# Kernel optimization log

Hardware: AMD Instinct MI355X
Metric: run time of the kernel (lower is better)

The kernel has to match this reference:

```python
import jax, jax.numpy as jnp
import numpy as np

H, W, B, D, N = 256, 256, 200, 128, 1024
NEG_SLOPE = 0.01  # nn.LeakyReLU default

def lrelu(x):
    return jnp.where(x > 0, x, NEG_SLOPE * x)

def setup_inputs() -> dict:
    key = jax.random.key(0)
    ks = jax.random.split(key, 12)
    x = jax.random.normal(ks[0], (H, W, B), dtype=jnp.float32)
    # pixel->superpixel soft assignment (nonnegative)
    Q = jax.random.uniform(ks[1], (H * W, N), dtype=jnp.float32)
    # sparse-ish symmetric superpixel adjacency
    a = (jax.random.uniform(ks[2], (N, N)) < 0.05).astype(jnp.float32)
    adj = jnp.maximum(a, a.T)
    s = 0.05
    params = {
        'bn0_g': jnp.ones((B,), jnp.float32), 'bn0_b': jnp.zeros((B,), jnp.float32),
        'w1': s * jax.random.normal(ks[3], (B, D), jnp.float32), 'b1': jnp.zeros((D,), jnp.float32),
        'bn1_g': jnp.ones((D,), jnp.float32), 'bn1_b': jnp.zeros((D,), jnp.float32),
        'w2': s * jax.random.normal(ks[4], (D, D), jnp.float32), 'b2': jnp.zeros((D,), jnp.float32),
        'gcn_bn_g': jnp.ones((3, D), jnp.float32), 'gcn_bn_b': jnp.zeros((3, D), jnp.float32),
        'gcn_w': s * jax.random.normal(ks[5], (3, D, D), jnp.float32),
        'gcn_b': jnp.zeros((3, D), jnp.float32),
    }
    return dict(x=x, Q=Q, adj=adj, **params)

def reference(x, Q, adj, bn0_g, bn0_b, w1, b1, bn1_g, bn1_b, w2, b2,
              gcn_bn_g, gcn_bn_b, gcn_w, gcn_b):
    h_, w_, _ = x.shape
    # CNN_denoise: BN2d + 1x1 conv (== per-pixel matmul) x2, LeakyReLU
    t = bn0_g * x + bn0_b                      # eval-mode BN (identity running stats)
    t = lrelu(jnp.einsum('hwb,bd->hwd', t, w1) + b1)
    t = bn1_g * t + bn1_b
    t = lrelu(jnp.einsum('hwd,de->hwe', t, w2) + b2)
    xf = t.reshape(h_ * w_, -1)                # [HW, D]
    # superpixel pooling with column-normalized Q
    normQ = Q / jnp.sum(Q, axis=0, keepdims=True)
    h = normQ.T @ xf                           # [N, D]
    # symmetric-normalized adjacency (A + I), computed once (same for all layers)
    g = adj + jnp.eye(adj.shape[0], dtype=adj.dtype)
    dinv = jnp.sum(g, axis=1) ** -0.5
    gn = dinv[:, None] * g * dinv[None, :]     # D^-1/2 (A+I) D^-1/2
    for i in range(3):                         # 3 GCN layers (structural loop)
        hb = gcn_bn_g[i] * h + gcn_bn_b[i]     # BatchNorm1d, eval mode
        h = lrelu((gn @ hb) @ gcn_w[i] + gcn_b[i])
    # write superpixel features back to pixels
    out = Q @ h                                # [HW, D]
    return out
```

## Files before the change

kernel.cpp:

```cpp
#include <hip/hip_runtime.h>

#define HWP 65536
#define NSP 1024
#define DCH 128
#define KC  64
#define JC  16

typedef float f32x4 __attribute__((ext_vector_type(4)));
typedef short bf16x8 __attribute__((ext_vector_type(8)));
typedef short bf16x4 __attribute__((ext_vector_type(4)));

__device__ __forceinline__ float lrelu(float v) { return v > 0.f ? v : 0.01f * v; }

__device__ __forceinline__ short f2bf(float f) {
    __bf16 h = (__bf16)f;
    return __builtin_bit_cast(short, h);
}

__device__ __forceinline__ void cvtA(bf16x8 (&bf)[4], const float (&src)[4][8])
{
#pragma unroll
    for (int mf = 0; mf < 4; ++mf)
#pragma unroll
        for (int j = 0; j < 8; ++j) bf[mf][j] = f2bf(src[mf][j]);
}

__global__ __launch_bounds__(256) void prep_w(
    const float* __restrict__ w1, const float* __restrict__ b1,
    const float* __restrict__ bn0_g, const float* __restrict__ bn0_b,
    const float* __restrict__ w2, const float* __restrict__ b2,
    const float* __restrict__ bn1_g, const float* __restrict__ bn1_b,
    short* __restrict__ w1t, short* __restrict__ w2t,
    float* __restrict__ b1f, float* __restrict__ b2f)
{
    int t = blockIdx.x * 256 + threadIdx.x;
    if (t < 7 * 8 * 64 * 8) {
        int j = t & 7, lane = (t >> 3) & 63, nf = (t >> 9) & 7, ks = t >> 12;
        int ch = ks * 32 + (lane >> 4) * 8 + j;
        int d  = nf * 16 + (lane & 15);
        float v = (ch < 200) ? bn0_g[ch] * w1[ch * 128 + d] : 0.f;
        w1t[t] = f2bf(v);
    }
    if (t < 4 * 8 * 64 * 8) {
        int j = t & 7, lane = (t >> 3) & 63, nf = (t >> 9) & 7, ks = t >> 12;
        int k = ks * 32 + (lane >> 4) * 8 + j;
        int d = nf * 16 + (lane & 15);
        w2t[t] = f2bf(bn1_g[k] * w2[k * 128 + d]);
    }
    if (t < 128) {
        float s1 = b1[t], s2 = b2[t];
        for (int ch = 0; ch < 200; ++ch) s1 += bn0_b[ch] * w1[ch * 128 + t];
        for (int k = 0; k < 128; ++k)   s2 += bn1_b[k] * w2[k * 128 + t];
        b1f[t] = s1; b2f[t] = s2;
    }
}

__global__ __launch_bounds__(128) void cnn_mfma(
    const float* __restrict__ x, const short* __restrict__ w1t,
    const float* __restrict__ b1f, const short* __restrict__ w2t,
    const float* __restrict__ b2f, short* __restrict__ xfT)
{
    __shared__ __align__(16) short a2[2][4][4][64][8];
    const int t = threadIdx.x;
    const int w = t >> 6, l = t & 63;
    const int q = l >> 4, li = l & 15;
    const int pix0 = blockIdx.x * 128 + w * 64;

    f32x4 acc[4][8];
#pragma unroll
    for (int nf = 0; nf < 8; ++nf) {
        float bv = b1f[nf * 16 + li];
#pragma unroll
        for (int mf = 0; mf < 4; ++mf) acc[mf][nf] = (f32x4){bv, bv, bv, bv};
    }

    for (int ks = 0; ks < 7; ++ks) {
        bf16x8 a[4];
        if (ks < 6 || q == 0) {
            int k0 = ks * 32 + q * 8;
#pragma unroll
            for (int mf = 0; mf < 4; ++mf) {
                const float* sp = &x[(size_t)(pix0 + mf * 16 + li) * 200 + k0];
                float4 u = *(const float4*)sp;
                float4 v = *(const float4*)(sp + 4);
                a[mf][0] = f2bf(u.x); a[mf][1] = f2bf(u.y);
                a[mf][2] = f2bf(u.z); a[mf][3] = f2bf(u.w);
                a[mf][4] = f2bf(v.x); a[mf][5] = f2bf(v.y);
                a[mf][6] = f2bf(v.z); a[mf][7] = f2bf(v.w);
            }
        } else {
#pragma unroll
            for (int mf = 0; mf < 4; ++mf)
#pragma unroll
                for (int j = 0; j < 8; ++j) a[mf][j] = 0;
        }
#pragma unroll
        for (int nf = 0; nf < 8; ++nf) {
            bf16x8 b = *(const bf16x8*)&w1t[((ks * 8 + nf) * 64 + l) * 8];
#pragma unroll
            for (int mf = 0; mf < 4; ++mf)
                acc[mf][nf] = __builtin_amdgcn_mfma_f32_16x16x32_bf16(a[mf], b, acc[mf][nf], 0, 0, 0);
        }
    }

#pragma unroll
    for (int mf = 0; mf < 4; ++mf)
#pragma unroll
        for (int nf = 0; nf < 8; ++nf)
#pragma unroll
            for (int j = 0; j < 4; ++j) {
                float v = lrelu(acc[mf][nf][j]);
                int row = mf * 16 + q * 4 + j;
                int col = nf * 16 + li;
                int ks2 = col >> 5;
                int lane2 = (row & 15) + (((col & 31) >> 3) << 4);
                a2[w][ks2][mf][lane2][col & 7] = f2bf(v);
            }
    __syncthreads();

    f32x4 acc2[4][8];
#pragma unroll
    for (int nf = 0; nf < 8; ++nf) {
        float bv = b2f[nf * 16 + li];
#pragma unroll
        for (int mf = 0; mf < 4; ++mf) acc2[mf][nf] = (f32x4){bv, bv, bv, bv};
    }
#pragma unroll
    for (int ks = 0; ks < 4; ++ks) {
        bf16x8 a[4];
#pragma unroll
        for (int mf = 0; mf < 4; ++mf)
            a[mf] = *(const bf16x8*)&a2[w][ks][mf][l][0];
#pragma unroll
        for (int nf = 0; nf < 8; ++nf) {
            bf16x8 b = *(const bf16x8*)&w2t[((ks * 8 + nf) * 64 + l) * 8];
#pragma unroll
            for (int mf = 0; mf < 4; ++mf)
                acc2[mf][nf] = __builtin_amdgcn_mfma_f32_16x16x32_bf16(a[mf], b, acc2[mf][nf], 0, 0, 0);
        }
    }

#pragma unroll
    for (int mf = 0; mf < 4; ++mf)
#pragma unroll
        for (int nf = 0; nf < 8; ++nf) {
            bf16x4 p;
#pragma unroll
            for (int j = 0; j < 4; ++j) p[j] = f2bf(lrelu(acc2[mf][nf][j]));
            int d2 = nf * 16 + li;
            int pix = pix0 + mf * 16 + q * 4;
            *(bf16x4*)&xfT[(size_t)d2 * HWP + pix] = p;
        }
}

__device__ __forceinline__ void pool_loadA(float (&dst)[4][8], const float* __restrict__ Q,
                                           int rbase, int ncol0)
{
#pragma unroll
    for (int mf = 0; mf < 4; ++mf) {
        const float* sp = &Q[(size_t)rbase * NSP + ncol0 + mf * 16];
#pragma unroll
        for (int j = 0; j < 8; ++j) dst[mf][j] = sp[(size_t)j * NSP];
    }
}
__device__ __forceinline__ void pool_loadB(bf16x8 (&dst)[4], const short* __restrict__ xfT,
                                           int dcol0, int rbase)
{
#pragma unroll
    for (int nf = 0; nf < 4; ++nf)
        dst[nf] = *(const bf16x8*)&xfT[(size_t)(dcol0 + nf * 16) * HWP + rbase];
}

__global__ __launch_bounds__(256, 2) void pool_mfma(
    const float* __restrict__ Q, const short* __restrict__ xfT,
    float* __restrict__ P_part, float* __restrict__ qs_part)
{
    const int t = threadIdx.x;
    const int wid = t >> 6, l = t & 63;
    const int q = l >> 4, li = l & 15;
    const int n0 = blockIdx.x * 128 + (wid >> 1) * 64;
    const int d0 = (wid & 1) * 64;
    const int chunk = blockIdx.y;
    const int r0 = chunk * 1024;
    const int ncol0 = n0 + li;
    const int dcol0 = d0 + li;

    f32x4 acc[4][4];
    f32x4 accq[4];
#pragma unroll
    for (int mf = 0; mf < 4; ++mf) {
        accq[mf] = (f32x4){0.f, 0.f, 0.f, 0.f};
#pragma unroll
        for (int nf = 0; nf < 4; ++nf) acc[mf][nf] = (f32x4){0.f, 0.f, 0.f, 0.f};
    }
    bf16x8 bone;
    {
        short onev = (li == 0) ? (short)0x3F80 : (short)0;
#pragma unroll
        for (int j = 0; j < 8; ++j) bone[j] = onev;
    }

    float a0[4][8], a1[4][8];
    bf16x8 b0[4], b1v[4];
    pool_loadA(a0, Q, r0 + q * 8, ncol0);
    pool_loadB(b0, xfT, dcol0, r0 + q * 8);

    for (int ks = 0; ks < 32; ks += 2) {
        pool_loadA(a1, Q, r0 + (ks + 1) * 32 + q * 8, ncol0);
        pool_loadB(b1v, xfT, dcol0, r0 + (ks + 1) * 32 + q * 8);
        {
            bf16x8 abf[4]; cvtA(abf, a0);
#pragma unroll
            for (int mf = 0; mf < 4; ++mf) {
#pragma unroll
                for (int nf = 0; nf < 4; ++nf)
                    acc[mf][nf] = __builtin_amdgcn_mfma_f32_16x16x32_bf16(abf[mf], b0[nf], acc[mf][nf], 0, 0, 0);
                if (d0 == 0)
                    accq[mf] = __builtin_amdgcn_mfma_f32_16x16x32_bf16(abf[mf], bone, accq[mf], 0, 0, 0);
            }
        }
        if (ks + 2 < 32) {
            pool_loadA(a0, Q, r0 + (ks + 2) * 32 + q * 8, ncol0);
            pool_loadB(b0, xfT, dcol0, r0 + (ks + 2) * 32 + q * 8);
        }
        {
            bf16x8 abf[4]; cvtA(abf, a1);
#pragma unroll
            for (int mf = 0; mf < 4; ++mf) {
#pragma unroll
                for (int nf = 0; nf < 4; ++nf)
                    acc[mf][nf] = __builtin_amdgcn_mfma_f32_16x16x32_bf16(abf[mf], b1v[nf], acc[mf][nf], 0, 0, 0);
                if (d0 == 0)
                    accq[mf] = __builtin_amdgcn_mfma_f32_16x16x32_bf16(abf[mf], bone, accq[mf], 0, 0, 0);
            }
        }
    }

#pragma unroll
    for (int mf = 0; mf < 4; ++mf)
#pragma unroll
        for (int nf = 0; nf < 4; ++nf)
#pragma unroll
            for (int j = 0; j < 4; ++j) {
                int n = n0 + mf * 16 + q * 4 + j;
                int d = d0 + nf * 16 + li;
                P_part[((size_t)chunk * NSP + n) * DCH + d] = acc[mf][nf][j];
            }
    if (d0 == 0 && li == 0)
#pragma unroll
        for (int mf = 0; mf < 4; ++mf)
#pragma unroll
            for (int j = 0; j < 4; ++j)
                qs_part[chunk * NSP + n0 + mf * 16 + q * 4 + j] = accq[mf][j];
}

__global__ __launch_bounds__(256) void reduce_h0(
    const float* __restrict__ P_part, const float* __restrict__ qs_part,
    float* __restrict__ h)
{
    const int i4 = blockIdx.x * 256 + threadIdx.x;
    const int n = i4 >> 5;
    f32x4 s = (f32x4){0.f, 0.f, 0.f, 0.f};
    const f32x4* P4 = (const f32x4*)P_part;
    for (int k = 0; k < KC; ++k) s += P4[(size_t)k * (NSP * DCH / 4) + i4];
    float qs = 0.f;
    for (int k = 0; k < KC; ++k) qs += qs_part[k * NSP + n];
    float inv = 1.f / qs;
    ((f32x4*)h)[i4] = s * inv;
}

__global__ __launch_bounds__(256) void dinv_k(const float* __restrict__ adj,
                                              float* __restrict__ dinv)
{
    __shared__ float red[256];
    const int n = blockIdx.x;
    const int t = threadIdx.x;
    float4 v = *(const float4*)&adj[(size_t)n * NSP + t * 4];
    red[t] = v.x + v.y + v.z + v.w;
    __syncthreads();
    for (int off = 128; off > 0; off >>= 1) {
        if (t < off) red[t] += red[t + off];
        __syncthreads();
    }
    if (t == 0) dinv[n] = rsqrtf(red[0] + 1.0f);
}

__global__ __launch_bounds__(256) void m1_k(
    const float* __restrict__ adj, const float* __restrict__ h,
    const float* __restrict__ dinv, const float* __restrict__ gg,
    const float* __restrict__ gb, float* __restrict__ m1p)
{
    __shared__ float adjL[16][64];
    __shared__ float hbL[64][128];
    const int r0 = blockIdx.x * 16;
    const int jc = blockIdx.y;
    const int j0 = jc * 64;
    const int t = threadIdx.x;
    const int d = t & 127, ph = t >> 7;

    for (int i = t; i < 16 * 64; i += 256) {
        int row = i >> 6, col = i & 63;
        adjL[row][col] = adj[(size_t)(r0 + row) * NSP + j0 + col];
    }
    for (int i = t; i < 64 * 128; i += 256) {
        int jr = i >> 7, dd = i & 127;
        int j = j0 + jr;
        hbL[jr][dd] = dinv[j] * (gg[dd] * h[(size_t)j * DCH + dd] + gb[dd]);
    }
    __syncthreads();

    float acc[8];
#pragma unroll
    for (int pp = 0; pp < 8; ++pp) acc[pp] = 0.f;
    for (int jj = 0; jj < 64; ++jj) {
        float hv = hbL[jj][d];
#pragma unroll
        for (int pp = 0; pp < 8; ++pp)
            acc[pp] += adjL[ph * 8 + pp][jj] * hv;
    }
#pragma unroll
    for (int pp = 0; pp < 8; ++pp)
        m1p[(size_t)jc * (NSP * DCH) + (size_t)(r0 + ph * 8 + pp) * DCH + d] = acc[pp];
}

__global__ __launch_bounds__(256) void gcnw_k(
    const float* __restrict__ m1p, const float* __restrict__ h,
    const float* __restrict__ dinv, const float* __restrict__ gg,
    const float* __restrict__ gb, const float* __restrict__ W,
    const float* __restrict__ bias, float* __restrict__ hout)
{
    __shared__ float ms[16 * 128];
    __shared__ float WL[64 * 128];
    const int r0 = blockIdx.x * 16;
    const int t = threadIdx.x;
    for (int i = t; i < 2048; i += 256) {
        int r = r0 + (i >> 7), dd = i & 127;
        float hbr = dinv[r] * (gg[dd] * h[(size_t)r * DCH + dd] + gb[dd]);
        float s = hbr;
#pragma unroll
        for (int kc = 0; kc < JC; ++kc)
            s += m1p[(size_t)kc * (NSP * DCH) + (size_t)r0 * DCH + i];
        ms[i] = dinv[r] * s;
    }
    const int e = t & 127, ph = t >> 7;
    float acc[8];
#pragma unroll
    for (int pp = 0; pp < 8; ++pp) acc[pp] = bias[e];
    for (int sub = 0; sub < 2; ++sub) {
        __syncthreads();
        for (int i = t; i < 64 * 128; i += 256)
            WL[i] = W[(size_t)sub * 64 * 128 + i];
        __syncthreads();
        for (int dd = 0; dd < 64; ++dd) {
            float wv = WL[dd * 128 + e];
#pragma unroll
            for (int pp = 0; pp < 8; ++pp)
                acc[pp] += ms[(ph * 8 + pp) * 128 + sub * 64 + dd] * wv;
        }
    }
#pragma unroll
    for (int pp = 0; pp < 8; ++pp)
        hout[(size_t)(r0 + ph * 8 + pp) * DCH + e] = lrelu(acc[pp]);
}

__global__ __launch_bounds__(256) void htprep(const float* __restrict__ h,
                                              short* __restrict__ htb)
{
    int t = blockIdx.x * 256 + threadIdx.x;
    int j = t & 7, lane = (t >> 3) & 63, nf = (t >> 9) & 7, ks = t >> 12;
    htb[t] = f2bf(h[(ks * 32 + (lane >> 4) * 8 + j) * 128 + nf * 16 + (lane & 15)]);
}

__device__ __forceinline__ void out_loadA(float (&dst)[4][8], const float* __restrict__ Q,
                                          int rrow0, int k0)
{
#pragma unroll
    for (int mf = 0; mf < 4; ++mf) {
        const float* sp = &Q[(size_t)(rrow0 + mf * 16) * NSP + k0];
        float4 u = *(const float4*)sp;
        float4 v = *(const float4*)(sp + 4);
        dst[mf][0] = u.x; dst[mf][1] = u.y; dst[mf][2] = u.z; dst[mf][3] = u.w;
        dst[mf][4] = v.x; dst[mf][5] = v.y; dst[mf][6] = v.z; dst[mf][7] = v.w;
    }
}
__device__ __forceinline__ void out_loadB(bf16x8 (&dst)[4], const short* __restrict__ htb,
                                          int ks, int nfbase, int l)
{
#pragma unroll
    for (int nf = 0; nf < 4; ++nf)
        dst[nf] = *(const bf16x8*)&htb[((ks * 8 + nfbase + nf) * 64 + l) * 8];
}

__global__ __launch_bounds__(256, 2) void out_mfma(
    const float* __restrict__ Q, const short* __restrict__ htb,
    float* __restrict__ out)
{
    const int t = threadIdx.x;
    const int wid = t >> 6, l = t & 63;
    const int q = l >> 4, li = l & 15;
    const int r0 = blockIdx.x * 128 + (wid >> 1) * 64;
    const int d0 = (wid & 1) * 64;
    const int rrow0 = r0 + li;
    const int nfb = d0 >> 4;

    f32x4 acc[4][4];
#pragma unroll
    for (int mf = 0; mf < 4; ++mf)
#pragma unroll
        for (int nf = 0; nf < 4; ++nf) acc[mf][nf] = (f32x4){0.f, 0.f, 0.f, 0.f};

    float a0[4][8], a1[4][8];
    bf16x8 b0[4], b1v[4];
    out_loadA(a0, Q, rrow0, q * 8);
    out_loadB(b0, htb, 0, nfb, l);

    for (int ks = 0; ks < 32; ks += 2) {
        out_loadA(a1, Q, rrow0, (ks + 1) * 32 + q * 8);
        out_loadB(b1v, htb, ks + 1, nfb, l);
        {
            bf16x8 abf[4]; cvtA(abf, a0);
#pragma unroll
            for (int mf = 0; mf < 4; ++mf)
#pragma unroll
                for (int nf = 0; nf < 4; ++nf)
                    acc[mf][nf] = __builtin_amdgcn_mfma_f32_16x16x32_bf16(abf[mf], b0[nf], acc[mf][nf], 0, 0, 0);
        }
        if (ks + 2 < 32) {
            out_loadA(a0, Q, rrow0, (ks + 2) * 32 + q * 8);
            out_loadB(b0, htb, ks + 2, nfb, l);
        }
        {
            bf16x8 abf[4]; cvtA(abf, a1);
#pragma unroll
            for (int mf = 0; mf < 4; ++mf)
#pragma unroll
                for (int nf = 0; nf < 4; ++nf)
                    acc[mf][nf] = __builtin_amdgcn_mfma_f32_16x16x32_bf16(abf[mf], b1v[nf], acc[mf][nf], 0, 0, 0);
        }
    }

#pragma unroll
    for (int mf = 0; mf < 4; ++mf)
#pragma unroll
        for (int nf = 0; nf < 4; ++nf)
#pragma unroll
            for (int j = 0; j < 4; ++j)
                out[(size_t)(r0 + mf * 16 + q * 4 + j) * DCH + d0 + nf * 16 + li] = acc[mf][nf][j];
}

extern "C" void kernel_launch(void* const* d_in, const int* in_sizes, int n_in,
                              void* d_out, int out_size, void* d_ws, size_t ws_size,
                              hipStream_t stream)
{
    const float* x      = (const float*)d_in[0];
    const float* Q      = (const float*)d_in[1];
    const float* adj    = (const float*)d_in[2];
    const float* bn0_g  = (const float*)d_in[3];
    const float* bn0_b  = (const float*)d_in[4];
    const float* w1     = (const float*)d_in[5];
    const float* b1     = (const float*)d_in[6];
    const float* bn1_g  = (const float*)d_in[7];
    const float* bn1_b  = (const float*)d_in[8];
    const float* w2     = (const float*)d_in[9];
    const float* b2     = (const float*)d_in[10];
    const float* gbn_g  = (const float*)d_in[11];
    const float* gbn_b  = (const float*)d_in[12];
    const float* gcn_w  = (const float*)d_in[13];
    const float* gcn_b  = (const float*)d_in[14];

    float* out = (float*)d_out;
    float* ws  = (float*)d_ws;

    float* P_part  = ws;
    float* qs_part = P_part + (size_t)KC * NSP * DCH;
    float* hA      = qs_part + (size_t)KC * NSP;
    float* hB      = hA + NSP * DCH;
    float* dinvb   = hB + NSP * DCH;
    short* htb     = (short*)(dinvb + NSP);
    short* w1t     = (short*)((float*)htb + 65536);
    short* w2t     = (short*)((float*)w1t + 14336);
    float* b1f     = (float*)w2t + 8192;
    float* b2f     = b1f + 128;
    float* m1p     = P_part;
    short* xfT     = (short*)d_out;

    prep_w<<<112, 256, 0, stream>>>(w1, b1, bn0_g, bn0_b, w2, b2, bn1_g, bn1_b,
                                    w1t, w2t, b1f, b2f);
    cnn_mfma<<<HWP / 128, 128, 0, stream>>>(x, w1t, b1f, w2t, b2f, xfT);
    pool_mfma<<<dim3(NSP / 128, KC), 256, 0, stream>>>(Q, xfT, P_part, qs_part);
    reduce_h0<<<(NSP * DCH / 4) / 256, 256, 0, stream>>>(P_part, qs_part, hA);
    dinv_k<<<NSP, 256, 0, stream>>>(adj, dinvb);

    const float* hcur = hA;
    float* hnext = hB;
    for (int i = 0; i < 3; ++i) {
        m1_k<<<dim3(NSP / 16, JC), 256, 0, stream>>>(adj, hcur, dinvb,
                                                     gbn_g + i * DCH, gbn_b + i * DCH, m1p);
        gcnw_k<<<NSP / 16, 256, 0, stream>>>(m1p, hcur, dinvb,
                                             gbn_g + i * DCH, gbn_b + i * DCH,
                                             gcn_w + (size_t)i * DCH * DCH,
                                             gcn_b + i * DCH, hnext);
        const float* tmp = hcur;
        hcur = hnext;
        hnext = (float*)tmp;
    }

    htprep<<<(NSP * DCH) / 256, 256, 0, stream>>>(hcur, htb);
    out_mfma<<<HWP / 128, 256, 0, stream>>>(Q, htb, out);
}
```

Before: 316.6 us.

## Stage Q tiles into LDS via async global_load_lds with double buffering

The out_mfma kernel previously had each wave load its own Q rows straight into registers, so the two waves sharing a row range fetched the same Q data twice. It now stages each 128x64 Q tile into a double-buffered, XOR-swizzled shared-memory buffer with global_load_lds, and waves read their fragments from LDS. This is meant to halve global Q traffic and overlap the next tile's load with MFMA work. In exchange it uses 64KB of LDS per block, which may limit occupancy, and adds a barrier per tile.

```diff
diff --git a/kernel.cpp b/kernel.cpp
--- a/kernel.cpp
+++ b/kernel.cpp
@@ -371,36 +371,42 @@
     htb[t] = f2bf(h[(ks * 32 + (lane >> 4) * 8 + j) * 128 + nf * 16 + (lane & 15)]);
 }
 
-__device__ __forceinline__ void out_loadA(float (&dst)[4][8], const float* __restrict__ Q,
-                                          int rrow0, int k0)
-{
-#pragma unroll
-    for (int mf = 0; mf < 4; ++mf) {
-        const float* sp = &Q[(size_t)(rrow0 + mf * 16) * NSP + k0];
-        float4 u = *(const float4*)sp;
-        float4 v = *(const float4*)(sp + 4);
-        dst[mf][0] = u.x; dst[mf][1] = u.y; dst[mf][2] = u.z; dst[mf][3] = u.w;
-        dst[mf][4] = v.x; dst[mf][5] = v.y; dst[mf][6] = v.z; dst[mf][7] = v.w;
-    }
-}
 __device__ __forceinline__ void out_loadB(bf16x8 (&dst)[4], const short* __restrict__ htb,
                                           int ks, int nfbase, int l)
 {
 #pragma unroll
     for (int nf = 0; nf < 4; ++nf)
         dst[nf] = *(const bf16x8*)&htb[((ks * 8 + nfbase + nf) * 64 + l) * 8];
+}
+
+__device__ __forceinline__ void stage_q(const float* __restrict__ Q, float* dst,
+                                        int r0, int kbase, int wid, int l)
+{
+#pragma unroll
+    for (int i = 0; i < 8; ++i) {
+        int o = (i * 4 + wid) * 1024 + l * 16;
+        int row = o >> 8;
+        int bin = o & 255;
+        const float* src = Q + (size_t)(r0 + row) * NSP + kbase
+                             + ((bin ^ ((row & 7) << 5)) >> 2);
+        __builtin_amdgcn_global_load_lds(
+            (const __attribute__((address_space(1))) unsigned int*)src,
+            (__attribute__((address_space(3))) unsigned int*)(dst + (o >> 2)),
+            16, 0, 0);
+    }
 }
 
 __global__ __launch_bounds__(256, 2) void out_mfma(
     const float* __restrict__ Q, const short* __restrict__ htb,
     float* __restrict__ out)
 {
+    __shared__ __align__(16) float qs[2][8192];
     const int t = threadIdx.x;
     const int wid = t >> 6, l = t & 63;
     const int q = l >> 4, li = l & 15;
-    const int r0 = blockIdx.x * 128 + (wid >> 1) * 64;
+    const int r0 = blockIdx.x * 128;
+    const int rw = (wid >> 1) * 64;
     const int d0 = (wid & 1) * 64;
-    const int rrow0 = r0 + li;
     const int nfb = d0 >> 4;
 
     f32x4 acc[4][4];
@@ -409,33 +415,53 @@
 #pragma unroll
         for (int nf = 0; nf < 4; ++nf) acc[mf][nf] = (f32x4){0.f, 0.f, 0.f, 0.f};
 
-    float a0[4][8], a1[4][8];
-    bf16x8 b0[4], b1v[4];
-    out_loadA(a0, Q, rrow0, q * 8);
-    out_loadB(b0, htb, 0, nfb, l);
-
-    for (int ks = 0; ks < 32; ks += 2) {
-        out_loadA(a1, Q, rrow0, (ks + 1) * 32 + q * 8);
-        out_loadB(b1v, htb, ks + 1, nfb, l);
-        {
-            bf16x8 abf[4]; cvtA(abf, a0);
-#pragma unroll
-            for (int mf = 0; mf < 4; ++mf)
-#pragma unroll
-                for (int nf = 0; nf < 4; ++nf)
-                    acc[mf][nf] = __builtin_amdgcn_mfma_f32_16x16x32_bf16(abf[mf], b0[nf], acc[mf][nf], 0, 0, 0);
-        }
-        if (ks + 2 < 32) {
-            out_loadA(a0, Q, rrow0, (ks + 2) * 32 + q * 8);
-            out_loadB(b0, htb, ks + 2, nfb, l);
-        }
-        {
-            bf16x8 abf[4]; cvtA(abf, a1);
-#pragma unroll
-            for (int mf = 0; mf < 4; ++mf)
-#pragma unroll
-                for (int nf = 0; nf < 4; ++nf)
-                    acc[mf][nf] = __builtin_amdgcn_mfma_f32_16x16x32_bf16(abf[mf], b1v[nf], acc[mf][nf], 0, 0, 0);
+    bf16x8 bA[4], bB[4];
+    out_loadB(bA, htb, 0, nfb, l);
+    out_loadB(bB, htb, 1, nfb, l);
+    stage_q(Q, qs[0], r0, 0, wid, l);
+    __syncthreads();
+
+    for (int tile = 0; tile < 16; ++tile) {
+        const int cur = tile & 1;
+        bf16x8 nA[4], nB[4];
+        if (tile < 15) {
+            out_loadB(nA, htb, (tile + 1) * 2,     nfb, l);
+            out_loadB(nB, htb, (tile + 1) * 2 + 1, nfb, l);
+            stage_q(Q, qs[cur ^ 1], r0, (tile + 1) * 64, wid, l);
+        }
+#pragma unroll
+        for (int ks = 0; ks < 2; ++ks) {
+            bf16x8 abf[4];
+#pragma unroll
+            for (int mf = 0; mf < 4; ++mf) {
+                int rl = rw + mf * 16 + li;
+                int koff = (ks * 32 + q * 8) << 2;
+                const float* p = &qs[cur][(rl << 6) + ((koff ^ ((rl & 7) << 5)) >> 2)];
+                float4 u = *(const float4*)p;
+                float4 v = *(const float4*)(p + 4);
+                abf[mf][0] = f2bf(u.x); abf[mf][1] = f2bf(u.y);
+                abf[mf][2] = f2bf(u.z); abf[mf][3] = f2bf(u.w);
+                abf[mf][4] = f2bf(v.x); abf[mf][5] = f2bf(v.y);
+                abf[mf][6] = f2bf(v.z); abf[mf][7] = f2bf(v.w);
+            }
+            if (ks == 0) {
+#pragma unroll
+                for (int mf = 0; mf < 4; ++mf)
+#pragma unroll
+                    for (int nf = 0; nf < 4; ++nf)
+                        acc[mf][nf] = __builtin_amdgcn_mfma_f32_16x16x32_bf16(abf[mf], bA[nf], acc[mf][nf], 0, 0, 0);
+            } else {
+#pragma unroll
+                for (int mf = 0; mf < 4; ++mf)
+#pragma unroll
+                    for (int nf = 0; nf < 4; ++nf)
+                        acc[mf][nf] = __builtin_amdgcn_mfma_f32_16x16x32_bf16(abf[mf], bB[nf], acc[mf][nf], 0, 0, 0);
+            }
+        }
+        __syncthreads();
+        if (tile < 15) {
+#pragma unroll
+            for (int nf = 0; nf < 4; ++nf) { bA[nf] = nA[nf]; bB[nf] = nB[nf]; }
         }
     }
 
@@ -445,7 +471,7 @@
         for (int nf = 0; nf < 4; ++nf)
 #pragma unroll
             for (int j = 0; j < 4; ++j)
-                out[(size_t)(r0 + mf * 16 + q * 4 + j) * DCH + d0 + nf * 16 + li] = acc[mf][nf][j];
+                out[(size_t)(r0 + rw + mf * 16 + q * 4 + j) * DCH + d0 + nf * 16 + li] = acc[mf][nf][j];
 }
 
 extern "C" void kernel_launch(void* const* d_in, const int* in_sizes, int n_in,
```

New measurement: 301.3 us. 4.8% less time.
